# Optimization experiments

Measured on AMD Instinct MI355X. Metric: run time of the kernel, lower is better.

The kernel has to match this reference:

```python
import jax, jax.numpy as jnp
import numpy as np
import math

N, S, D, V = 8, 2048, 64, 64

def setup_inputs() -> dict:
    key = jax.random.key(0)
    k1, k2, k3, k4 = jax.random.split(key, 4)
    return {
        "queries_nqd": jax.random.normal(k1, (N, S, D), dtype=jnp.float32),
        "keys_nsd": jax.random.normal(k2, (N, S, D), dtype=jnp.float32),
        "values_nsv": jax.random.normal(k3, (N, S, V), dtype=jnp.float32),
        "prefix_len_n": jax.random.randint(k4, (N,), 0, S, dtype=jnp.int64) if jax.config.jax_enable_x64 else jax.random.randint(k4, (N,), 0, S, dtype=jnp.int32),
    }

def reference(queries_nqd, keys_nsd, values_nsv, prefix_len_n):
    n, q, d = queries_nqd.shape
    s = keys_nsd.shape[1]
    # block mask: key position < prefix_len (broadcast over query dim)  [n, q, s]
    s_idx = jnp.arange(s)
    block_mask = s_idx[None, None, :] < prefix_len_n[:, None, None]
    # diagonal mask: q == s index  [q, s]
    diag_mask = s_idx[:, None] == s_idx[None, :]
    attention_mask_nqs = block_mask | diag_mask[None, :, :]
    scores_nqs = jnp.einsum("nqd,nsd->nqs", queries_nqd, keys_nsd) / math.sqrt(d)
    scores_nqs = jnp.where(attention_mask_nqs, scores_nqs, jnp.float32(-1e9))
    probs_nqs = jax.nn.softmax(scores_nqs, axis=-1)
    # dropout p=0.0 (eval/identity)
    return jnp.einsum("nqs,nsv->nqv", probs_nqs, values_nsv)
```

## Files before the change

kernel.cpp:

```cpp
#include <hip/hip_runtime.h>
#include <cstdint>
#include <cstddef>

typedef __attribute__((ext_vector_type(8))) __bf16 bf16x8;
typedef __attribute__((ext_vector_type(2))) __bf16 bf16x2;
typedef __attribute__((ext_vector_type(4))) float f32x4;
typedef __attribute__((ext_vector_type(4))) unsigned int u32x4;

#define LOG2E 1.44269504088896340736f

constexpr int N_ = 8;
constexpr int S_ = 2048;
constexpr int D_ = 64;
constexpr int V_ = 64;
constexpr int TQ = 32;
constexpr int CK = 64;
constexpr int NW = 4;

#define GLD(d, a, OFF) \
    asm volatile("global_load_dwordx4 %0, %1, off offset:" OFF : "=&v"(d) : "v"(a))
#define WAITV(N) do { asm volatile("s_waitcnt vmcnt(" #N ")" ::: "memory"); \
                      __builtin_amdgcn_sched_barrier(0); } while (0)

__device__ __forceinline__ ushort f2bf(float x) {
    uint u = __builtin_bit_cast(uint, x);
    return (ushort)((u + 0x7FFFu + ((u >> 16) & 1u)) >> 16);
}
__device__ __forceinline__ bf16x8 bc8(const u32x4& q) {
    return __builtin_bit_cast(bf16x8, q);
}
__device__ __forceinline__ bf16x8 cvt8(const float* p, float sc) {
    f32x4 a = *reinterpret_cast<const f32x4*>(p);
    f32x4 b = *reinterpret_cast<const f32x4*>(p + 4);
    bf16x8 r;
#pragma unroll
    for (int j = 0; j < 4; j++) { r[j] = (__bf16)(a[j] * sc); r[j + 4] = (__bf16)(b[j] * sc); }
    return r;
}
__device__ __forceinline__ uint pk2(float lo, float hi) {
    bf16x2 t; t[0] = (__bf16)lo; t[1] = (__bf16)hi;
    return __builtin_bit_cast(uint, t);
}

__device__ __forceinline__ int load_prefix(const int* plen, int n) {
    bool is64 = ((plen[1] | plen[3] | plen[5] | plen[7]) == 0);
    return is64 ? plen[2 * n] : plen[n];
}

__global__ void prep_kernel(const float* __restrict__ Q, const float* __restrict__ K,
                            const float* __restrict__ V, ushort* __restrict__ Qb,
                            ushort* __restrict__ Kb, ushort* __restrict__ VTb) {
    const float QS = 0.125f * LOG2E;
    const int i4 = (blockIdx.x * 256 + threadIdx.x) * 4;
    f32x4 q = *reinterpret_cast<const f32x4*>(Q + i4);
    f32x4 k = *reinterpret_cast<const f32x4*>(K + i4);
    f32x4 v = *reinterpret_cast<const f32x4*>(V + i4);
    ushort4 qo, ko;
    qo.x = f2bf(q[0] * QS); qo.y = f2bf(q[1] * QS); qo.z = f2bf(q[2] * QS); qo.w = f2bf(q[3] * QS);
    ko.x = f2bf(k[0]); ko.y = f2bf(k[1]); ko.z = f2bf(k[2]); ko.w = f2bf(k[3]);
    *reinterpret_cast<ushort4*>(Qb + i4) = qo;
    *reinterpret_cast<ushort4*>(Kb + i4) = ko;
    const int vd = i4 & (V_ - 1);
    const int s  = (i4 >> 6) & (S_ - 1);
    const int n  = i4 >> 17;
    const size_t base = ((size_t)n * 64 + (s >> 5)) * 2048 + (s & 31);
#pragma unroll
    for (int j = 0; j < 4; j++)
        VTb[base + (size_t)(vd + j) * 32] = f2bf(v[j]);
}

template <bool WS>
__global__ __launch_bounds__(256, 2) void attn_kernel(
    const void* __restrict__ Qp, const void* __restrict__ Kp,
    const void* __restrict__ Vp, const ushort* __restrict__ VTb,
    const int* __restrict__ plen, float* __restrict__ outm)
{
    __shared__ float obuf[NW][TQ][V_ + 1];
    __shared__ float lbuf[NW][TQ];

    const int n    = blockIdx.y;
    const int q0   = blockIdx.x * TQ;
    const int tid  = threadIdx.x;
    const int w    = tid >> 6;
    const int lane = tid & 63;
    const int quad = lane >> 4;
    const int l16  = lane & 15;
    const int prefix = load_prefix(plen, n);
    const int qrow0 = q0 + l16;
    const int qrow1 = q0 + 16 + l16;

    const int krow = ((l16 >> 2) << 3) + (l16 & 3);

    bf16x8 qf00, qf01, qf10, qf11;
    if (WS) {
        const ushort* qptr = (const ushort*)Qp + ((size_t)(n * S_ + qrow0)) * D_ + quad * 8;
        uint4 u0 = *reinterpret_cast<const uint4*>(qptr);
        uint4 u1 = *reinterpret_cast<const uint4*>(qptr + 32);
        uint4 u2 = *reinterpret_cast<const uint4*>(qptr + 16 * D_);
        uint4 u3 = *reinterpret_cast<const uint4*>(qptr + 16 * D_ + 32);
        qf00 = __builtin_bit_cast(bf16x8, u0); qf01 = __builtin_bit_cast(bf16x8, u1);
        qf10 = __builtin_bit_cast(bf16x8, u2); qf11 = __builtin_bit_cast(bf16x8, u3);
    } else {
        const float* qptr = (const float*)Qp + ((size_t)(n * S_ + qrow0)) * D_ + quad * 8;
        qf00 = cvt8(qptr, 0.125f * LOG2E);            qf01 = cvt8(qptr + 32, 0.125f * LOG2E);
        qf10 = cvt8(qptr + 16 * D_, 0.125f * LOG2E);  qf11 = cvt8(qptr + 16 * D_ + 32, 0.125f * LOG2E);
    }
    asm volatile("" : "+v"(qf00), "+v"(qf01), "+v"(qf10), "+v"(qf11));

    f32x4 oa[4], ob[4];
#pragma unroll
    for (int vb = 0; vb < 4; vb++) { oa[vb] = (f32x4){0.f,0.f,0.f,0.f}; ob[vb] = (f32x4){0.f,0.f,0.f,0.f}; }
    float l0 = 0.f, l1 = 0.f;

    const float* Kf = (const float*)Kp + (size_t)n * S_ * D_;
    const float* Vf = (const float*)Vp + (size_t)n * S_ * V_;

    const uint64_t kbase0 = (uint64_t)(uintptr_t)((const ushort*)Kp)
        + (size_t)n * S_ * D_ * 2 + (size_t)krow * 128 + quad * 16;
    const uint64_t vbase0 = (uint64_t)(uintptr_t)VTb
        + (size_t)n * 64 * 2048 * 2 + (size_t)l16 * 64 + quad * 16;

    auto issueKV = [&](u32x4* f, int c) {
        const uint64_t ka = kbase0 + (uint64_t)c * (CK * 128);
        const uint64_t kb = ka + 4096;
        const uint64_t va = vbase0 + (uint64_t)c * (2 * 4096);
        const uint64_t vb = va + 4096;
        GLD(f[0],  ka, "0");   GLD(f[1],  ka, "64");
        GLD(f[2],  ka, "512"); GLD(f[3],  ka, "576");
        GLD(f[4],  kb, "0");   GLD(f[5],  kb, "64");
        GLD(f[6],  kb, "512"); GLD(f[7],  kb, "576");
        GLD(f[8],  va, "0");   GLD(f[9],  va, "1024");
        GLD(f[10], va, "2048");GLD(f[11], va, "3072");
        GLD(f[12], vb, "0");   GLD(f[13], vb, "1024");
        GLD(f[14], vb, "2048");GLD(f[15], vb, "3072");
    };

    auto computeChunk = [&](const u32x4* f, int kb, bool masked, bool wait16) {
        const f32x4 zero = (f32x4){0.f, 0.f, 0.f, 0.f};
        uint4 pw0, pw1, pw2, pw3;
        {
            f32x4 s0 = __builtin_amdgcn_mfma_f32_16x16x32_bf16(bc8(f[0]), qf00, zero, 0, 0, 0);
            s0 = __builtin_amdgcn_mfma_f32_16x16x32_bf16(bc8(f[1]), qf01, s0, 0, 0, 0);
            f32x4 s1 = __builtin_amdgcn_mfma_f32_16x16x32_bf16(bc8(f[2]), qf00, zero, 0, 0, 0);
            s1 = __builtin_amdgcn_mfma_f32_16x16x32_bf16(bc8(f[3]), qf01, s1, 0, 0, 0);
            f32x4 s2 = __builtin_amdgcn_mfma_f32_16x16x32_bf16(bc8(f[4]), qf00, zero, 0, 0, 0);
            s2 = __builtin_amdgcn_mfma_f32_16x16x32_bf16(bc8(f[5]), qf01, s2, 0, 0, 0);
            f32x4 s3 = __builtin_amdgcn_mfma_f32_16x16x32_bf16(bc8(f[6]), qf00, zero, 0, 0, 0);
            s3 = __builtin_amdgcn_mfma_f32_16x16x32_bf16(bc8(f[7]), qf01, s3, 0, 0, 0);
            if (masked) {
#pragma unroll
                for (int r = 0; r < 4; r++) {
                    const int k0 = kb + 8 * quad + r;
                    s0[r] = (k0      < prefix || k0      == qrow0) ? s0[r] : -1e30f;
                    s1[r] = (k0 + 4  < prefix || k0 + 4  == qrow0) ? s1[r] : -1e30f;
                    s2[r] = (k0 + 32 < prefix || k0 + 32 == qrow0) ? s2[r] : -1e30f;
                    s3[r] = (k0 + 36 < prefix || k0 + 36 == qrow0) ? s3[r] : -1e30f;
                }
            }
            float p0[4], p1[4], p2[4], p3[4];
#pragma unroll
            for (int r = 0; r < 4; r++) {
                p0[r] = __builtin_amdgcn_exp2f(s0[r]);
                p1[r] = __builtin_amdgcn_exp2f(s1[r]);
                p2[r] = __builtin_amdgcn_exp2f(s2[r]);
                p3[r] = __builtin_amdgcn_exp2f(s3[r]);
            }
            l0 += ((p0[0]+p0[1])+(p0[2]+p0[3])) + ((p1[0]+p1[1])+(p1[2]+p1[3]))
                + ((p2[0]+p2[1])+(p2[2]+p2[3])) + ((p3[0]+p3[1])+(p3[2]+p3[3]));
            pw0.x = pk2(p0[0], p0[1]); pw0.y = pk2(p0[2], p0[3]);
            pw0.z = pk2(p1[0], p1[1]); pw0.w = pk2(p1[2], p1[3]);
            pw1.x = pk2(p2[0], p2[1]); pw1.y = pk2(p2[2], p2[3]);
            pw1.z = pk2(p3[0], p3[1]); pw1.w = pk2(p3[2], p3[3]);
        }
        {
            f32x4 s0 = __builtin_amdgcn_mfma_f32_16x16x32_bf16(bc8(f[0]), qf10, zero, 0, 0, 0);
            s0 = __builtin_amdgcn_mfma_f32_16x16x32_bf16(bc8(f[1]), qf11, s0, 0, 0, 0);
            f32x4 s1 = __builtin_amdgcn_mfma_f32_16x16x32_bf16(bc8(f[2]), qf10, zero, 0, 0, 0);
            s1 = __builtin_amdgcn_mfma_f32_16x16x32_bf16(bc8(f[3]), qf11, s1, 0, 0, 0);
            f32x4 s2 = __builtin_amdgcn_mfma_f32_16x16x32_bf16(bc8(f[4]), qf10, zero, 0, 0, 0);
            s2 = __builtin_amdgcn_mfma_f32_16x16x32_bf16(bc8(f[5]), qf11, s2, 0, 0, 0);
            f32x4 s3 = __builtin_amdgcn_mfma_f32_16x16x32_bf16(bc8(f[6]), qf10, zero, 0, 0, 0);
            s3 = __builtin_amdgcn_mfma_f32_16x16x32_bf16(bc8(f[7]), qf11, s3, 0, 0, 0);
            if (masked) {
#pragma unroll
                for (int r = 0; r < 4; r++) {
                    const int k0 = kb + 8 * quad + r;
                    s0[r] = (k0      < prefix || k0      == qrow1) ? s0[r] : -1e30f;
                    s1[r] = (k0 + 4  < prefix || k0 + 4  == qrow1) ? s1[r] : -1e30f;
                    s2[r] = (k0 + 32 < prefix || k0 + 32 == qrow1) ? s2[r] : -1e30f;
                    s3[r] = (k0 + 36 < prefix || k0 + 36 == qrow1) ? s3[r] : -1e30f;
                }
            }
            float p0[4], p1[4], p2[4], p3[4];
#pragma unroll
            for (int r = 0; r < 4; r++) {
                p0[r] = __builtin_amdgcn_exp2f(s0[r]);
                p1[r] = __builtin_amdgcn_exp2f(s1[r]);
                p2[r] = __builtin_amdgcn_exp2f(s2[r]);
                p3[r] = __builtin_amdgcn_exp2f(s3[r]);
            }
            l1 += ((p0[0]+p0[1])+(p0[2]+p0[3])) + ((p1[0]+p1[1])+(p1[2]+p1[3]))
                + ((p2[0]+p2[1])+(p2[2]+p2[3])) + ((p3[0]+p3[1])+(p3[2]+p3[3]));
            pw2.x = pk2(p0[0], p0[1]); pw2.y = pk2(p0[2], p0[3]);
            pw2.z = pk2(p1[0], p1[1]); pw2.w = pk2(p1[2], p1[3]);
            pw3.x = pk2(p2[0], p2[1]); pw3.y = pk2(p2[2], p2[3]);
            pw3.z = pk2(p3[0], p3[1]); pw3.w = pk2(p3[2], p3[3]);
        }
        if (wait16) WAITV(16);
        const bf16x8 pA0 = __builtin_bit_cast(bf16x8, pw0);
        const bf16x8 pA1 = __builtin_bit_cast(bf16x8, pw1);
        const bf16x8 pB0 = __builtin_bit_cast(bf16x8, pw2);
        const bf16x8 pB1 = __builtin_bit_cast(bf16x8, pw3);
#pragma unroll
        for (int vb = 0; vb < 4; vb++) {
            oa[vb] = __builtin_amdgcn_mfma_f32_16x16x32_bf16(bc8(f[8 + vb]),  pA0, oa[vb], 0, 0, 0);
            oa[vb] = __builtin_amdgcn_mfma_f32_16x16x32_bf16(bc8(f[12 + vb]), pA1, oa[vb], 0, 0, 0);
            ob[vb] = __builtin_amdgcn_mfma_f32_16x16x32_bf16(bc8(f[8 + vb]),  pB0, ob[vb], 0, 0, 0);
            ob[vb] = __builtin_amdgcn_mfma_f32_16x16x32_bf16(bc8(f[12 + vb]), pB1, ob[vb], 0, 0, 0);
        }
    };

    const int nFull = prefix >> 6;
    const int nPC   = (prefix + CK - 1) >> 6;
    const int dc    = q0 >> 6;

    if (WS) {
        u32x4 bufA[16], bufB[16];
        int c = w;
        if (c < nFull) {
            issueKV(bufA, c);
            int c1 = c + NW;
            if (c1 >= nFull) {
                WAITV(0); computeChunk(bufA, c * CK, false, false);
            } else {
                issueKV(bufB, c1);
                for (;;) {
                    int c2 = c1 + NW;
                    if (c2 >= nFull) {
                        WAITV(16); computeChunk(bufA, c * CK, false, false);
                        WAITV(0);  computeChunk(bufB, c1 * CK, false, false);
                        break;
                    }
                    WAITV(24);
                    computeChunk(bufA, c * CK, false, true);
                    issueKV(bufA, c2);
                    c = c1; c1 = c2; c2 = c1 + NW;
                    if (c2 >= nFull) {
                        WAITV(16); computeChunk(bufB, c * CK, false, false);
                        WAITV(0);  computeChunk(bufA, c1 * CK, false, false);
                        break;
                    }
                    WAITV(24);
                    computeChunk(bufB, c * CK, false, true);
                    issueKV(bufB, c2);
                    c = c1; c1 = c2;
                }
            }
        }
        if (nPC > nFull && (nFull & (NW - 1)) == w) {
            issueKV(bufA, nFull); WAITV(0); computeChunk(bufA, nFull * CK, true, false);
        }
        if (dc >= nPC && (dc & (NW - 1)) == w) {
            issueKV(bufA, dc); WAITV(0); computeChunk(bufA, dc * CK, true, false);
        }
    } else {
        for (int c = w; c < nFull + 2; c++) {
            int cc; bool masked;
            if (c < nFull) { if ((c & (NW - 1)) != (w & (NW - 1)) || c >= nFull) {} }
            break;
        }
        auto computeNW = [&](int kb, bool masked) {
            u32x4 f[16];
            const float* kp = Kf + (size_t)(kb + krow) * D_ + quad * 8;
            f[0] = __builtin_bit_cast(u32x4, cvt8(kp, 1.f));
            f[1] = __builtin_bit_cast(u32x4, cvt8(kp + 32, 1.f));
            f[2] = __builtin_bit_cast(u32x4, cvt8(kp + 4 * D_, 1.f));
            f[3] = __builtin_bit_cast(u32x4, cvt8(kp + 4 * D_ + 32, 1.f));
            f[4] = __builtin_bit_cast(u32x4, cvt8(kp + 32 * D_, 1.f));
            f[5] = __builtin_bit_cast(u32x4, cvt8(kp + 32 * D_ + 32, 1.f));
            f[6] = __builtin_bit_cast(u32x4, cvt8(kp + 36 * D_, 1.f));
            f[7] = __builtin_bit_cast(u32x4, cvt8(kp + 36 * D_ + 32, 1.f));
#pragma unroll
            for (int vb = 0; vb < 4; vb++) {
                bf16x8 vf0, vf1;
#pragma unroll
                for (int j = 0; j < 8; j++) {
                    vf0[j] = (__bf16)Vf[(size_t)(kb + quad * 8 + j) * V_ + vb * 16 + l16];
                    vf1[j] = (__bf16)Vf[(size_t)(kb + 32 + quad * 8 + j) * V_ + vb * 16 + l16];
                }
                f[8 + vb]  = __builtin_bit_cast(u32x4, vf0);
                f[12 + vb] = __builtin_bit_cast(u32x4, vf1);
            }
            computeChunk(f, kb, masked, false);
        };
        for (int c = w; c < nFull; c += NW) computeNW(c * CK, false);
        if (nPC > nFull && (nFull & (NW - 1)) == w) computeNW(nFull * CK, true);
        if (dc >= nPC && (dc & (NW - 1)) == w) computeNW(dc * CK, true);
    }

#pragma unroll
    for (int vb = 0; vb < 4; vb++)
#pragma unroll
        for (int r = 0; r < 4; r++) {
            obuf[w][l16][vb * 16 + quad * 4 + r]      = oa[vb][r];
            obuf[w][16 + l16][vb * 16 + quad * 4 + r] = ob[vb][r];
        }
    l0 += __shfl_xor(l0, 16, 64);
    l0 += __shfl_xor(l0, 32, 64);
    l1 += __shfl_xor(l1, 16, 64);
    l1 += __shfl_xor(l1, 32, 64);
    if (quad == 0) { lbuf[w][l16] = l0; lbuf[w][16 + l16] = l1; }
    __syncthreads();

    const int row = tid >> 3;
    const int vd0 = (tid & 7) * 8;
    float lg = (lbuf[0][row] + lbuf[1][row]) + (lbuf[2][row] + lbuf[3][row]);
    float acc[8] = {0.f,0.f,0.f,0.f,0.f,0.f,0.f,0.f};
#pragma unroll
    for (int ww = 0; ww < NW; ww++) {
#pragma unroll
        for (int i = 0; i < 8; i++) acc[i] += obuf[ww][row][vd0 + i];
    }
    const float inv = 1.f / lg;
    f32x4 o4a = (f32x4){acc[0] * inv, acc[1] * inv, acc[2] * inv, acc[3] * inv};
    f32x4 o4b = (f32x4){acc[4] * inv, acc[5] * inv, acc[6] * inv, acc[7] * inv};
    float* op = outm + ((size_t)(n * S_ + q0 + row)) * V_ + vd0;
    *reinterpret_cast<f32x4*>(op)     = o4a;
    *reinterpret_cast<f32x4*>(op + 4) = o4b;
}

extern "C" void kernel_launch(void* const* d_in, const int* in_sizes, int n_in,
                              void* d_out, int out_size, void* d_ws, size_t ws_size,
                              hipStream_t stream) {
    const float* Qf = (const float*)d_in[0];
    const float* Kf = (const float*)d_in[1];
    const float* Vf = (const float*)d_in[2];
    const int* plen = (const int*)d_in[3];
    float* outm = (float*)d_out;

    constexpr size_t ELEMS = (size_t)N_ * S_ * D_;
    const size_t need = 3 * ELEMS * sizeof(ushort);
    dim3 agrid(S_ / TQ, N_);

    if (ws_size >= need) {
        ushort* Qb  = (ushort*)d_ws;
        ushort* Kb  = Qb + ELEMS;
        ushort* VTb = Kb + ELEMS;
        prep_kernel<<<ELEMS / (256 * 4), 256, 0, stream>>>(Qf, Kf, Vf, Qb, Kb, VTb);
        attn_kernel<true><<<agrid, 256, 0, stream>>>(Qb, Kb, nullptr, VTb, plen, outm);
    } else {
        attn_kernel<false><<<agrid, 256, 0, stream>>>(Qf, Kf, Vf, nullptr, plen, outm);
    }
}
```

Measured before the change: 91.46 us.

## Balance load by sorting batches by prefix and pairing tasks per block

The prep kernel now sorts the batch indices by prefix length and writes a task schedule. The attention kernel launches half as many blocks with 8 waves each, and each block handles two tasks: one from the front of the sorted list and one from the back, so long and short prefix workloads are paired. Global loads now use a scalar base with a 32-bit vector offset, which cuts address VGPR use. The cost is an extra barrier between the two tasks, a larger shared reduction buffer, and the loss of the 2D grid.

```diff
diff --git a/kernel.cpp b/kernel.cpp
--- a/kernel.cpp
+++ b/kernel.cpp
@@ -15,10 +15,12 @@
 constexpr int V_ = 64;
 constexpr int TQ = 32;
 constexpr int CK = 64;
-constexpr int NW = 4;
-
-#define GLD(d, a, OFF) \
-    asm volatile("global_load_dwordx4 %0, %1, off offset:" OFF : "=&v"(d) : "v"(a))
+constexpr int NW = 8;
+constexpr int NTASK = (S_ / TQ) * N_;
+
+#define GLDS(d, off, base, OFF) \
+    asm volatile("global_load_dwordx4 %0, %1, %2 offset:" OFF \
+                 : "=&v"(d) : "v"(off), "s"(base))
 #define WAITV(N) do { asm volatile("s_waitcnt vmcnt(" #N ")" ::: "memory"); \
                       __builtin_amdgcn_sched_barrier(0); } while (0)
 
@@ -49,7 +51,8 @@
 
 __global__ void prep_kernel(const float* __restrict__ Q, const float* __restrict__ K,
                             const float* __restrict__ V, ushort* __restrict__ Qb,
-                            ushort* __restrict__ Kb, ushort* __restrict__ VTb) {
+                            ushort* __restrict__ Kb, ushort* __restrict__ VTb,
+                            const int* __restrict__ plen, int* __restrict__ sched) {
     const float QS = 0.125f * LOG2E;
     const int i4 = (blockIdx.x * 256 + threadIdx.x) * 4;
     f32x4 q = *reinterpret_cast<const f32x4*>(Q + i4);
@@ -67,266 +70,288 @@
 #pragma unroll
     for (int j = 0; j < 4; j++)
         VTb[base + (size_t)(vd + j) * 32] = f2bf(v[j]);
+
+    if (blockIdx.x == 0) {
+        __shared__ int ordl[8];
+        if (threadIdx.x == 0) {
+            int pv[8];
+#pragma unroll
+            for (int i = 0; i < 8; i++) { pv[i] = load_prefix(plen, i); ordl[i] = i; }
+            for (int i = 1; i < 8; i++)
+                for (int j = i; j > 0 && pv[ordl[j]] > pv[ordl[j - 1]]; j--) {
+                    int t = ordl[j]; ordl[j] = ordl[j - 1]; ordl[j - 1] = t;
+                }
+        }
+        __syncthreads();
+        for (int t = threadIdx.x; t < NTASK; t += 256)
+            sched[t] = (ordl[t >> 6] << 16) | (t & 63);
+    }
 }
 
 template <bool WS>
-__global__ __launch_bounds__(256, 2) void attn_kernel(
+__global__ __launch_bounds__(512, 2) void attn_kernel(
     const void* __restrict__ Qp, const void* __restrict__ Kp,
     const void* __restrict__ Vp, const ushort* __restrict__ VTb,
-    const int* __restrict__ plen, float* __restrict__ outm)
+    const int* __restrict__ plen, const int* __restrict__ sched,
+    float* __restrict__ outm)
 {
     __shared__ float obuf[NW][TQ][V_ + 1];
     __shared__ float lbuf[NW][TQ];
 
-    const int n    = blockIdx.y;
-    const int q0   = blockIdx.x * TQ;
     const int tid  = threadIdx.x;
     const int w    = tid >> 6;
     const int lane = tid & 63;
     const int quad = lane >> 4;
     const int l16  = lane & 15;
-    const int prefix = load_prefix(plen, n);
-    const int qrow0 = q0 + l16;
-    const int qrow1 = q0 + 16 + l16;
-
     const int krow = ((l16 >> 2) << 3) + (l16 & 3);
-
-    bf16x8 qf00, qf01, qf10, qf11;
-    if (WS) {
-        const ushort* qptr = (const ushort*)Qp + ((size_t)(n * S_ + qrow0)) * D_ + quad * 8;
-        uint4 u0 = *reinterpret_cast<const uint4*>(qptr);
-        uint4 u1 = *reinterpret_cast<const uint4*>(qptr + 32);
-        uint4 u2 = *reinterpret_cast<const uint4*>(qptr + 16 * D_);
-        uint4 u3 = *reinterpret_cast<const uint4*>(qptr + 16 * D_ + 32);
-        qf00 = __builtin_bit_cast(bf16x8, u0); qf01 = __builtin_bit_cast(bf16x8, u1);
-        qf10 = __builtin_bit_cast(bf16x8, u2); qf11 = __builtin_bit_cast(bf16x8, u3);
-    } else {
-        const float* qptr = (const float*)Qp + ((size_t)(n * S_ + qrow0)) * D_ + quad * 8;
-        qf00 = cvt8(qptr, 0.125f * LOG2E);            qf01 = cvt8(qptr + 32, 0.125f * LOG2E);
-        qf10 = cvt8(qptr + 16 * D_, 0.125f * LOG2E);  qf11 = cvt8(qptr + 16 * D_ + 32, 0.125f * LOG2E);
+    const uint vk0 = (uint)(krow * 128 + quad * 16);
+    const uint vv0 = (uint)(l16 * 64 + quad * 16);
+
+    const int nIt = WS ? 2 : 1;
+    for (int it = 0; it < nIt; it++) {
+        int n, q0;
+        if (WS) {
+            const int entry = sched[it == 0 ? (int)blockIdx.x
+                                            : (NTASK - 1 - (int)blockIdx.x)];
+            n  = entry >> 16;
+            q0 = (entry & 0xffff) * TQ;
+        } else {
+            n  = blockIdx.y;
+            q0 = blockIdx.x * TQ;
+        }
+        __syncthreads();
+
+        const int prefix = load_prefix(plen, n);
+        const int qrow0 = q0 + l16;
+        const int qrow1 = q0 + 16 + l16;
+
+        bf16x8 qf00, qf01, qf10, qf11;
+        if (WS) {
+            const ushort* qptr = (const ushort*)Qp + ((size_t)(n * S_ + qrow0)) * D_ + quad * 8;
+            uint4 u0 = *reinterpret_cast<const uint4*>(qptr);
+            uint4 u1 = *reinterpret_cast<const uint4*>(qptr + 32);
+            uint4 u2 = *reinterpret_cast<const uint4*>(qptr + 16 * D_);
+            uint4 u3 = *reinterpret_cast<const uint4*>(qptr + 16 * D_ + 32);
+            qf00 = __builtin_bit_cast(bf16x8, u0); qf01 = __builtin_bit_cast(bf16x8, u1);
+            qf10 = __builtin_bit_cast(bf16x8, u2); qf11 = __builtin_bit_cast(bf16x8, u3);
+        } else {
+            const float* qptr = (const float*)Qp + ((size_t)(n * S_ + qrow0)) * D_ + quad * 8;
+            qf00 = cvt8(qptr, 0.125f * LOG2E);            qf01 = cvt8(qptr + 32, 0.125f * LOG2E);
+            qf10 = cvt8(qptr + 16 * D_, 0.125f * LOG2E);  qf11 = cvt8(qptr + 16 * D_ + 32, 0.125f * LOG2E);
+        }
+        asm volatile("" : "+v"(qf00), "+v"(qf01), "+v"(qf10), "+v"(qf11));
+
+        f32x4 oa[4], ob[4];
+#pragma unroll
+        for (int vb = 0; vb < 4; vb++) { oa[vb] = (f32x4){0.f,0.f,0.f,0.f}; ob[vb] = (f32x4){0.f,0.f,0.f,0.f}; }
+        float l0 = 0.f, l1 = 0.f;
+
+        const float* Kf = (const float*)Kp + (size_t)n * S_ * D_;
+        const float* Vf = (const float*)Vp + (size_t)n * S_ * V_;
+        const ushort* Kbb = (const ushort*)Kp + (size_t)n * S_ * D_;
+        const ushort* VTn = VTb + (size_t)n * 64 * 2048;
+
+        auto issueKV = [&](u32x4* f, int c) {
+            const uint ko  = vk0 + (uint)c * 8192u;
+            const uint ko2 = ko + 4096u;
+            const uint vo  = vv0 + (uint)c * 8192u;
+            const uint vo2 = vo + 4096u;
+            GLDS(f[0],  ko,  Kbb, "0");    GLDS(f[1],  ko,  Kbb, "64");
+            GLDS(f[2],  ko,  Kbb, "512");  GLDS(f[3],  ko,  Kbb, "576");
+            GLDS(f[4],  ko2, Kbb, "0");    GLDS(f[5],  ko2, Kbb, "64");
+            GLDS(f[6],  ko2, Kbb, "512");  GLDS(f[7],  ko2, Kbb, "576");
+            GLDS(f[8],  vo,  VTn, "0");    GLDS(f[9],  vo,  VTn, "1024");
+            GLDS(f[10], vo,  VTn, "2048"); GLDS(f[11], vo,  VTn, "3072");
+            GLDS(f[12], vo2, VTn, "0");    GLDS(f[13], vo2, VTn, "1024");
+            GLDS(f[14], vo2, VTn, "2048"); GLDS(f[15], vo2, VTn, "3072");
+        };
+
+        auto computeChunk = [&](const u32x4* f, int kb, bool masked, bool wait16) {
+            const f32x4 zero = (f32x4){0.f, 0.f, 0.f, 0.f};
+            uint4 pw0, pw1, pw2, pw3;
+            {
+                f32x4 s0 = __builtin_amdgcn_mfma_f32_16x16x32_bf16(bc8(f[0]), qf00, zero, 0, 0, 0);
+                s0 = __builtin_amdgcn_mfma_f32_16x16x32_bf16(bc8(f[1]), qf01, s0, 0, 0, 0);
+                f32x4 s1 = __builtin_amdgcn_mfma_f32_16x16x32_bf16(bc8(f[2]), qf00, zero, 0, 0, 0);
+                s1 = __builtin_amdgcn_mfma_f32_16x16x32_bf16(bc8(f[3]), qf01, s1, 0, 0, 0);
+                f32x4 s2 = __builtin_amdgcn_mfma_f32_16x16x32_bf16(bc8(f[4]), qf00, zero, 0, 0, 0);
+                s2 = __builtin_amdgcn_mfma_f32_16x16x32_bf16(bc8(f[5]), qf01, s2, 0, 0, 0);
+                f32x4 s3 = __builtin_amdgcn_mfma_f32_16x16x32_bf16(bc8(f[6]), qf00, zero, 0, 0, 0);
+                s3 = __builtin_amdgcn_mfma_f32_16x16x32_bf16(bc8(f[7]), qf01, s3, 0, 0, 0);
+                if (masked) {
+#pragma unroll
+                    for (int r = 0; r < 4; r++) {
+                        const int k0 = kb + 8 * quad + r;
+                        s0[r] = (k0      < prefix || k0      == qrow0) ? s0[r] : -1e30f;
+                        s1[r] = (k0 + 4  < prefix || k0 + 4  == qrow0) ? s1[r] : -1e30f;
+                        s2[r] = (k0 + 32 < prefix || k0 + 32 == qrow0) ? s2[r] : -1e30f;
+                        s3[r] = (k0 + 36 < prefix || k0 + 36 == qrow0) ? s3[r] : -1e30f;
+                    }
+                }
+                float p0[4], p1[4], p2[4], p3[4];
+#pragma unroll
+                for (int r = 0; r < 4; r++) {
+                    p0[r] = __builtin_amdgcn_exp2f(s0[r]);
+                    p1[r] = __builtin_amdgcn_exp2f(s1[r]);
+                    p2[r] = __builtin_amdgcn_exp2f(s2[r]);
+                    p3[r] = __builtin_amdgcn_exp2f(s3[r]);
+                }
+                l0 += ((p0[0]+p0[1])+(p0[2]+p0[3])) + ((p1[0]+p1[1])+(p1[2]+p1[3]))
+                    + ((p2[0]+p2[1])+(p2[2]+p2[3])) + ((p3[0]+p3[1])+(p3[2]+p3[3]));
+                pw0.x = pk2(p0[0], p0[1]); pw0.y = pk2(p0[2], p0[3]);
+                pw0.z = pk2(p1[0], p1[1]); pw0.w = pk2(p1[2], p1[3]);
+                pw1.x = pk2(p2[0], p2[1]); pw1.y = pk2(p2[2], p2[3]);
+                pw1.z = pk2(p3[0], p3[1]); pw1.w = pk2(p3[2], p3[3]);
+            }
+            {
+                f32x4 s0 = __builtin_amdgcn_mfma_f32_16x16x32_bf16(bc8(f[0]), qf10, zero, 0, 0, 0);
+                s0 = __builtin_amdgcn_mfma_f32_16x16x32_bf16(bc8(f[1]), qf11, s0, 0, 0, 0);
+                f32x4 s1 = __builtin_amdgcn_mfma_f32_16x16x32_bf16(bc8(f[2]), qf10, zero, 0, 0, 0);
+                s1 = __builtin_amdgcn_mfma_f32_16x16x32_bf16(bc8(f[3]), qf11, s1, 0, 0, 0);
+                f32x4 s2 = __builtin_amdgcn_mfma_f32_16x16x32_bf16(bc8(f[4]), qf10, zero, 0, 0, 0);
+                s2 = __builtin_amdgcn_mfma_f32_16x16x32_bf16(bc8(f[5]), qf11, s2, 0, 0, 0);
+                f32x4 s3 = __builtin_amdgcn_mfma_f32_16x16x32_bf16(bc8(f[6]), qf10, zero, 0, 0, 0);
+                s3 = __builtin_amdgcn_mfma_f32_16x16x32_bf16(bc8(f[7]), qf11, s3, 0, 0, 0);
+                if (masked) {
+#pragma unroll
+                    for (int r = 0; r < 4; r++) {
+                        const int k0 = kb + 8 * quad + r;
+                        s0[r] = (k0      < prefix || k0      == qrow1) ? s0[r] : -1e30f;
+                        s1[r] = (k0 + 4  < prefix || k0 + 4  == qrow1) ? s1[r] : -1e30f;
+                        s2[r] = (k0 + 32 < prefix || k0 + 32 == qrow1) ? s2[r] : -1e30f;
+                        s3[r] = (k0 + 36 < prefix || k0 + 36 == qrow1) ? s3[r] : -1e30f;
+                    }
+                }
+                float p0[4], p1[4], p2[4], p3[4];
+#pragma unroll
+                for (int r = 0; r < 4; r++) {
+                    p0[r] = __builtin_amdgcn_exp2f(s0[r]);
+                    p1[r] = __builtin_amdgcn_exp2f(s1[r]);
+                    p2[r] = __builtin_amdgcn_exp2f(s2[r]);
+                    p3[r] = __builtin_amdgcn_exp2f(s3[r]);
+                }
+                l1 += ((p0[0]+p0[1])+(p0[2]+p0[3])) + ((p1[0]+p1[1])+(p1[2]+p1[3]))
+                    + ((p2[0]+p2[1])+(p2[2]+p2[3])) + ((p3[0]+p3[1])+(p3[2]+p3[3]));
+                pw2.x = pk2(p0[0], p0[1]); pw2.y = pk2(p0[2], p0[3]);
+                pw2.z = pk2(p1[0], p1[1]); pw2.w = pk2(p1[2], p1[3]);
+                pw3.x = pk2(p2[0], p2[1]); pw3.y = pk2(p2[2], p2[3]);
+                pw3.z = pk2(p3[0], p3[1]); pw3.w = pk2(p3[2], p3[3]);
+            }
+            if (wait16) WAITV(16);
+            const bf16x8 pA0 = __builtin_bit_cast(bf16x8, pw0);
+            const bf16x8 pA1 = __builtin_bit_cast(bf16x8, pw1);
+            const bf16x8 pB0 = __builtin_bit_cast(bf16x8, pw2);
+            const bf16x8 pB1 = __builtin_bit_cast(bf16x8, pw3);
+#pragma unroll
+            for (int vb = 0; vb < 4; vb++) {
+                oa[vb] = __builtin_amdgcn_mfma_f32_16x16x32_bf16(bc8(f[8 + vb]),  pA0, oa[vb], 0, 0, 0);
+                oa[vb] = __builtin_amdgcn_mfma_f32_16x16x32_bf16(bc8(f[12 + vb]), pA1, oa[vb], 0, 0, 0);
+                ob[vb] = __builtin_amdgcn_mfma_f32_16x16x32_bf16(bc8(f[8 + vb]),  pB0, ob[vb], 0, 0, 0);
+                ob[vb] = __builtin_amdgcn_mfma_f32_16x16x32_bf16(bc8(f[12 + vb]), pB1, ob[vb], 0, 0, 0);
+            }
+        };
+
+        const int nFull = prefix >> 6;
+        const int nPC   = (prefix + CK - 1) >> 6;
+        const int dc    = q0 >> 6;
+
+        if (WS) {
+            u32x4 bufA[16], bufB[16];
+            int c = w;
+            if (c < nFull) {
+                issueKV(bufA, c);
+                int c1 = c + NW;
+                if (c1 >= nFull) {
+                    WAITV(0); computeChunk(bufA, c * CK, false, false);
+                } else {
+                    issueKV(bufB, c1);
+                    for (;;) {
+                        int c2 = c1 + NW;
+                        if (c2 >= nFull) {
+                            WAITV(16); computeChunk(bufA, c * CK, false, false);
+                            WAITV(0);  computeChunk(bufB, c1 * CK, false, false);
+                            break;
+                        }
+                        WAITV(24);
+                        computeChunk(bufA, c * CK, false, true);
+                        issueKV(bufA, c2);
+                        c = c1; c1 = c2; c2 = c1 + NW;
+                        if (c2 >= nFull) {
+                            WAITV(16); computeChunk(bufB, c * CK, false, false);
+                            WAITV(0);  computeChunk(bufA, c1 * CK, false, false);
+                            break;
+                        }
+                        WAITV(24);
+                        computeChunk(bufB, c * CK, false, true);
+                        issueKV(bufB, c2);
+                        c = c1; c1 = c2;
+                    }
+                }
+            }
+            if (nPC > nFull && (nFull & (NW - 1)) == w) {
+                issueKV(bufA, nFull); WAITV(0); computeChunk(bufA, nFull * CK, true, false);
+            }
+            if (dc >= nPC && (dc & (NW - 1)) == w) {
+                issueKV(bufA, dc); WAITV(0); computeChunk(bufA, dc * CK, true, false);
+            }
+        } else {
+            auto computeNW = [&](int kb, bool masked) {
+                u32x4 f[16];
+                const float* kp = Kf + (size_t)(kb + krow) * D_ + quad * 8;
+                f[0] = __builtin_bit_cast(u32x4, cvt8(kp, 1.f));
+                f[1] = __builtin_bit_cast(u32x4, cvt8(kp + 32, 1.f));
+                f[2] = __builtin_bit_cast(u32x4, cvt8(kp + 4 * D_, 1.f));
+                f[3] = __builtin_bit_cast(u32x4, cvt8(kp + 4 * D_ + 32, 1.f));
+                f[4] = __builtin_bit_cast(u32x4, cvt8(kp + 32 * D_, 1.f));
+                f[5] = __builtin_bit_cast(u32x4, cvt8(kp + 32 * D_ + 32, 1.f));
+                f[6] = __builtin_bit_cast(u32x4, cvt8(kp + 36 * D_, 1.f));
+                f[7] = __builtin_bit_cast(u32x4, cvt8(kp + 36 * D_ + 32, 1.f));
+#pragma unroll
+                for (int vb = 0; vb < 4; vb++) {
+                    bf16x8 vf0, vf1;
+#pragma unroll
+                    for (int j = 0; j < 8; j++) {
+                        vf0[j] = (__bf16)Vf[(size_t)(kb + quad * 8 + j) * V_ + vb * 16 + l16];
+                        vf1[j] = (__bf16)Vf[(size_t)(kb + 32 + quad * 8 + j) * V_ + vb * 16 + l16];
+                    }
+                    f[8 + vb]  = __builtin_bit_cast(u32x4, vf0);
+                    f[12 + vb] = __builtin_bit_cast(u32x4, vf1);
+                }
+                computeChunk(f, kb, masked, false);
+            };
+            for (int c = w; c < nFull; c += NW) computeNW(c * CK, false);
+            if (nPC > nFull && (nFull & (NW - 1)) == w) computeNW(nFull * CK, true);
+            if (dc >= nPC && (dc & (NW - 1)) == w) computeNW(dc * CK, true);
+        }
+
+#pragma unroll
+        for (int vb = 0; vb < 4; vb++)
+#pragma unroll
+            for (int r = 0; r < 4; r++) {
+                obuf[w][l16][vb * 16 + quad * 4 + r]      = oa[vb][r];
+                obuf[w][16 + l16][vb * 16 + quad * 4 + r] = ob[vb][r];
+            }
+        l0 += __shfl_xor(l0, 16, 64);
+        l0 += __shfl_xor(l0, 32, 64);
+        l1 += __shfl_xor(l1, 16, 64);
+        l1 += __shfl_xor(l1, 32, 64);
+        if (quad == 0) { lbuf[w][l16] = l0; lbuf[w][16 + l16] = l1; }
+        __syncthreads();
+
+        const int row = tid >> 4;
+        const int vd0 = (tid & 15) * 4;
+        float lg = 0.f;
+        float acc[4] = {0.f, 0.f, 0.f, 0.f};
+#pragma unroll
+        for (int ww = 0; ww < NW; ww++) {
+            lg += lbuf[ww][row];
+#pragma unroll
+            for (int i = 0; i < 4; i++) acc[i] += obuf[ww][row][vd0 + i];
+        }
+        const float inv = 1.f / lg;
+        f32x4 o4 = (f32x4){acc[0] * inv, acc[1] * inv, acc[2] * inv, acc[3] * inv};
+        *reinterpret_cast<f32x4*>(outm + ((size_t)(n * S_ + q0 + row)) * V_ + vd0) = o4;
     }
-    asm volatile("" : "+v"(qf00), "+v"(qf01), "+v"(qf10), "+v"(qf11));
-
-    f32x4 oa[4], ob[4];
-#pragma unroll
-    for (int vb = 0; vb < 4; vb++) { oa[vb] = (f32x4){0.f,0.f,0.f,0.f}; ob[vb] = (f32x4){0.f,0.f,0.f,0.f}; }
-    float l0 = 0.f, l1 = 0.f;
-
-    const float* Kf = (const float*)Kp + (size_t)n * S_ * D_;
-    const float* Vf = (const float*)Vp + (size_t)n * S_ * V_;
-
-    const uint64_t kbase0 = (uint64_t)(uintptr_t)((const ushort*)Kp)
-        + (size_t)n * S_ * D_ * 2 + (size_t)krow * 128 + quad * 16;
-    const uint64_t vbase0 = (uint64_t)(uintptr_t)VTb
-        + (size_t)n * 64 * 2048 * 2 + (size_t)l16 * 64 + quad * 16;
-
-    auto issueKV = [&](u32x4* f, int c) {
-        const uint64_t ka = kbase0 + (uint64_t)c * (CK * 128);
-        const uint64_t kb = ka + 4096;
-        const uint64_t va = vbase0 + (uint64_t)c * (2 * 4096);
-        const uint64_t vb = va + 4096;
-        GLD(f[0],  ka, "0");   GLD(f[1],  ka, "64");
-        GLD(f[2],  ka, "512"); GLD(f[3],  ka, "576");
-        GLD(f[4],  kb, "0");   GLD(f[5],  kb, "64");
-        GLD(f[6],  kb, "512"); GLD(f[7],  kb, "576");
-        GLD(f[8],  va, "0");   GLD(f[9],  va, "1024");
-        GLD(f[10], va, "2048");GLD(f[11], va, "3072");
-        GLD(f[12], vb, "0");   GLD(f[13], vb, "1024");
-        GLD(f[14], vb, "2048");GLD(f[15], vb, "3072");
-    };
-
-    auto computeChunk = [&](const u32x4* f, int kb, bool masked, bool wait16) {
-        const f32x4 zero = (f32x4){0.f, 0.f, 0.f, 0.f};
-        uint4 pw0, pw1, pw2, pw3;
-        {
-            f32x4 s0 = __builtin_amdgcn_mfma_f32_16x16x32_bf16(bc8(f[0]), qf00, zero, 0, 0, 0);
-            s0 = __builtin_amdgcn_mfma_f32_16x16x32_bf16(bc8(f[1]), qf01, s0, 0, 0, 0);
-            f32x4 s1 = __builtin_amdgcn_mfma_f32_16x16x32_bf16(bc8(f[2]), qf00, zero, 0, 0, 0);
-            s1 = __builtin_amdgcn_mfma_f32_16x16x32_bf16(bc8(f[3]), qf01, s1, 0, 0, 0);
-            f32x4 s2 = __builtin_amdgcn_mfma_f32_16x16x32_bf16(bc8(f[4]), qf00, zero, 0, 0, 0);
-            s2 = __builtin_amdgcn_mfma_f32_16x16x32_bf16(bc8(f[5]), qf01, s2, 0, 0, 0);
-            f32x4 s3 = __builtin_amdgcn_mfma_f32_16x16x32_bf16(bc8(f[6]), qf00, zero, 0, 0, 0);
-            s3 = __builtin_amdgcn_mfma_f32_16x16x32_bf16(bc8(f[7]), qf01, s3, 0, 0, 0);
-            if (masked) {
-#pragma unroll
-                for (int r = 0; r < 4; r++) {
-                    const int k0 = kb + 8 * quad + r;
-                    s0[r] = (k0      < prefix || k0      == qrow0) ? s0[r] : -1e30f;
-                    s1[r] = (k0 + 4  < prefix || k0 + 4  == qrow0) ? s1[r] : -1e30f;
-                    s2[r] = (k0 + 32 < prefix || k0 + 32 == qrow0) ? s2[r] : -1e30f;
-                    s3[r] = (k0 + 36 < prefix || k0 + 36 == qrow0) ? s3[r] : -1e30f;
-                }
-            }
-            float p0[4], p1[4], p2[4], p3[4];
-#pragma unroll
-            for (int r = 0; r < 4; r++) {
-                p0[r] = __builtin_amdgcn_exp2f(s0[r]);
-                p1[r] = __builtin_amdgcn_exp2f(s1[r]);
-                p2[r] = __builtin_amdgcn_exp2f(s2[r]);
-                p3[r] = __builtin_amdgcn_exp2f(s3[r]);
-            }
-            l0 += ((p0[0]+p0[1])+(p0[2]+p0[3])) + ((p1[0]+p1[1])+(p1[2]+p1[3]))
-                + ((p2[0]+p2[1])+(p2[2]+p2[3])) + ((p3[0]+p3[1])+(p3[2]+p3[3]));
-            pw0.x = pk2(p0[0], p0[1]); pw0.y = pk2(p0[2], p0[3]);
-            pw0.z = pk2(p1[0], p1[1]); pw0.w = pk2(p1[2], p1[3]);
-            pw1.x = pk2(p2[0], p2[1]); pw1.y = pk2(p2[2], p2[3]);
-            pw1.z = pk2(p3[0], p3[1]); pw1.w = pk2(p3[2], p3[3]);
-        }
-        {
-            f32x4 s0 = __builtin_amdgcn_mfma_f32_16x16x32_bf16(bc8(f[0]), qf10, zero, 0, 0, 0);
-            s0 = __builtin_amdgcn_mfma_f32_16x16x32_bf16(bc8(f[1]), qf11, s0, 0, 0, 0);
-            f32x4 s1 = __builtin_amdgcn_mfma_f32_16x16x32_bf16(bc8(f[2]), qf10, zero, 0, 0, 0);
-            s1 = __builtin_amdgcn_mfma_f32_16x16x32_bf16(bc8(f[3]), qf11, s1, 0, 0, 0);
-            f32x4 s2 = __builtin_amdgcn_mfma_f32_16x16x32_bf16(bc8(f[4]), qf10, zero, 0, 0, 0);
-            s2 = __builtin_amdgcn_mfma_f32_16x16x32_bf16(bc8(f[5]), qf11, s2, 0, 0, 0);
-            f32x4 s3 = __builtin_amdgcn_mfma_f32_16x16x32_bf16(bc8(f[6]), qf10, zero, 0, 0, 0);
-            s3 = __builtin_amdgcn_mfma_f32_16x16x32_bf16(bc8(f[7]), qf11, s3, 0, 0, 0);
-            if (masked) {
-#pragma unroll
-                for (int r = 0; r < 4; r++) {
-                    const int k0 = kb + 8 * quad + r;
-                    s0[r] = (k0      < prefix || k0      == qrow1) ? s0[r] : -1e30f;
-                    s1[r] = (k0 + 4  < prefix || k0 + 4  == qrow1) ? s1[r] : -1e30f;
-                    s2[r] = (k0 + 32 < prefix || k0 + 32 == qrow1) ? s2[r] : -1e30f;
-                    s3[r] = (k0 + 36 < prefix || k0 + 36 == qrow1) ? s3[r] : -1e30f;
-                }
-            }
-            float p0[4], p1[4], p2[4], p3[4];
-#pragma unroll
-            for (int r = 0; r < 4; r++) {
-                p0[r] = __builtin_amdgcn_exp2f(s0[r]);
-                p1[r] = __builtin_amdgcn_exp2f(s1[r]);
-                p2[r] = __builtin_amdgcn_exp2f(s2[r]);
-                p3[r] = __builtin_amdgcn_exp2f(s3[r]);
-            }
-            l1 += ((p0[0]+p0[1])+(p0[2]+p0[3])) + ((p1[0]+p1[1])+(p1[2]+p1[3]))
-                + ((p2[0]+p2[1])+(p2[2]+p2[3])) + ((p3[0]+p3[1])+(p3[2]+p3[3]));
-            pw2.x = pk2(p0[0], p0[1]); pw2.y = pk2(p0[2], p0[3]);
-            pw2.z = pk2(p1[0], p1[1]); pw2.w = pk2(p1[2], p1[3]);
-            pw3.x = pk2(p2[0], p2[1]); pw3.y = pk2(p2[2], p2[3]);
-            pw3.z = pk2(p3[0], p3[1]); pw3.w = pk2(p3[2], p3[3]);
-        }
-        if (wait16) WAITV(16);
-        const bf16x8 pA0 = __builtin_bit_cast(bf16x8, pw0);
-        const bf16x8 pA1 = __builtin_bit_cast(bf16x8, pw1);
-        const bf16x8 pB0 = __builtin_bit_cast(bf16x8, pw2);
-        const bf16x8 pB1 = __builtin_bit_cast(bf16x8, pw3);
-#pragma unroll
-        for (int vb = 0; vb < 4; vb++) {
-            oa[vb] = __builtin_amdgcn_mfma_f32_16x16x32_bf16(bc8(f[8 + vb]),  pA0, oa[vb], 0, 0, 0);
-            oa[vb] = __builtin_amdgcn_mfma_f32_16x16x32_bf16(bc8(f[12 + vb]), pA1, oa[vb], 0, 0, 0);
-            ob[vb] = __builtin_amdgcn_mfma_f32_16x16x32_bf16(bc8(f[8 + vb]),  pB0, ob[vb], 0, 0, 0);
-            ob[vb] = __builtin_amdgcn_mfma_f32_16x16x32_bf16(bc8(f[12 + vb]), pB1, ob[vb], 0, 0, 0);
-        }
-    };
-
-    const int nFull = prefix >> 6;
-    const int nPC   = (prefix + CK - 1) >> 6;
-    const int dc    = q0 >> 6;
-
-    if (WS) {
-        u32x4 bufA[16], bufB[16];
-        int c = w;
-        if (c < nFull) {
-            issueKV(bufA, c);
-            int c1 = c + NW;
-            if (c1 >= nFull) {
-                WAITV(0); computeChunk(bufA, c * CK, false, false);
-            } else {
-                issueKV(bufB, c1);
-                for (;;) {
-                    int c2 = c1 + NW;
-                    if (c2 >= nFull) {
-                        WAITV(16); computeChunk(bufA, c * CK, false, false);
-                        WAITV(0);  computeChunk(bufB, c1 * CK, false, false);
-                        break;
-                    }
-                    WAITV(24);
-                    computeChunk(bufA, c * CK, false, true);
-                    issueKV(bufA, c2);
-                    c = c1; c1 = c2; c2 = c1 + NW;
-                    if (c2 >= nFull) {
-                        WAITV(16); computeChunk(bufB, c * CK, false, false);
-                        WAITV(0);  computeChunk(bufA, c1 * CK, false, false);
-                        break;
-                    }
-                    WAITV(24);
-                    computeChunk(bufB, c * CK, false, true);
-                    issueKV(bufB, c2);
-                    c = c1; c1 = c2;
-                }
-            }
-        }
-        if (nPC > nFull && (nFull & (NW - 1)) == w) {
-            issueKV(bufA, nFull); WAITV(0); computeChunk(bufA, nFull * CK, true, false);
-        }
-        if (dc >= nPC && (dc & (NW - 1)) == w) {
-            issueKV(bufA, dc); WAITV(0); computeChunk(bufA, dc * CK, true, false);
-        }
-    } else {
-        for (int c = w; c < nFull + 2; c++) {
-            int cc; bool masked;
-            if (c < nFull) { if ((c & (NW - 1)) != (w & (NW - 1)) || c >= nFull) {} }
-            break;
-        }
-        auto computeNW = [&](int kb, bool masked) {
-            u32x4 f[16];
-            const float* kp = Kf + (size_t)(kb + krow) * D_ + quad * 8;
-            f[0] = __builtin_bit_cast(u32x4, cvt8(kp, 1.f));
-            f[1] = __builtin_bit_cast(u32x4, cvt8(kp + 32, 1.f));
-            f[2] = __builtin_bit_cast(u32x4, cvt8(kp + 4 * D_, 1.f));
-            f[3] = __builtin_bit_cast(u32x4, cvt8(kp + 4 * D_ + 32, 1.f));
-            f[4] = __builtin_bit_cast(u32x4, cvt8(kp + 32 * D_, 1.f));
-            f[5] = __builtin_bit_cast(u32x4, cvt8(kp + 32 * D_ + 32, 1.f));
-            f[6] = __builtin_bit_cast(u32x4, cvt8(kp + 36 * D_, 1.f));
-            f[7] = __builtin_bit_cast(u32x4, cvt8(kp + 36 * D_ + 32, 1.f));
-#pragma unroll
-            for (int vb = 0; vb < 4; vb++) {
-                bf16x8 vf0, vf1;
-#pragma unroll
-                for (int j = 0; j < 8; j++) {
-                    vf0[j] = (__bf16)Vf[(size_t)(kb + quad * 8 + j) * V_ + vb * 16 + l16];
-                    vf1[j] = (__bf16)Vf[(size_t)(kb + 32 + quad * 8 + j) * V_ + vb * 16 + l16];
-                }
-                f[8 + vb]  = __builtin_bit_cast(u32x4, vf0);
-                f[12 + vb] = __builtin_bit_cast(u32x4, vf1);
-            }
-            computeChunk(f, kb, masked, false);
-        };
-        for (int c = w; c < nFull; c += NW) computeNW(c * CK, false);
-        if (nPC > nFull && (nFull & (NW - 1)) == w) computeNW(nFull * CK, true);
-        if (dc >= nPC && (dc & (NW - 1)) == w) computeNW(dc * CK, true);
-    }
-
-#pragma unroll
-    for (int vb = 0; vb < 4; vb++)
-#pragma unroll
-        for (int r = 0; r < 4; r++) {
-            obuf[w][l16][vb * 16 + quad * 4 + r]      = oa[vb][r];
-            obuf[w][16 + l16][vb * 16 + quad * 4 + r] = ob[vb][r];
-        }
-    l0 += __shfl_xor(l0, 16, 64);
-    l0 += __shfl_xor(l0, 32, 64);
-    l1 += __shfl_xor(l1, 16, 64);
-    l1 += __shfl_xor(l1, 32, 64);
-    if (quad == 0) { lbuf[w][l16] = l0; lbuf[w][16 + l16] = l1; }
-    __syncthreads();
-
-    const int row = tid >> 3;
-    const int vd0 = (tid & 7) * 8;
-    float lg = (lbuf[0][row] + lbuf[1][row]) + (lbuf[2][row] + lbuf[3][row]);
-    float acc[8] = {0.f,0.f,0.f,0.f,0.f,0.f,0.f,0.f};
-#pragma unroll
-    for (int ww = 0; ww < NW; ww++) {
-#pragma unroll
-        for (int i = 0; i < 8; i++) acc[i] += obuf[ww][row][vd0 + i];
-    }
-    const float inv = 1.f / lg;
-    f32x4 o4a = (f32x4){acc[0] * inv, acc[1] * inv, acc[2] * inv, acc[3] * inv};
-    f32x4 o4b = (f32x4){acc[4] * inv, acc[5] * inv, acc[6] * inv, acc[7] * inv};
-    float* op = outm + ((size_t)(n * S_ + q0 + row)) * V_ + vd0;
-    *reinterpret_cast<f32x4*>(op)     = o4a;
-    *reinterpret_cast<f32x4*>(op + 4) = o4b;
 }
 
 extern "C" void kernel_launch(void* const* d_in, const int* in_sizes, int n_in,
@@ -339,16 +364,16 @@
     float* outm = (float*)d_out;
 
     constexpr size_t ELEMS = (size_t)N_ * S_ * D_;
-    const size_t need = 3 * ELEMS * sizeof(ushort);
-    dim3 agrid(S_ / TQ, N_);
+    const size_t need = 3 * ELEMS * sizeof(ushort) + NTASK * sizeof(int);
 
     if (ws_size >= need) {
         ushort* Qb  = (ushort*)d_ws;
         ushort* Kb  = Qb + ELEMS;
         ushort* VTb = Kb + ELEMS;
-        prep_kernel<<<ELEMS / (256 * 4), 256, 0, stream>>>(Qf, Kf, Vf, Qb, Kb, VTb);
-        attn_kernel<true><<<agrid, 256, 0, stream>>>(Qb, Kb, nullptr, VTb, plen, outm);
+        int*   sched = (int*)(VTb + ELEMS);
+        prep_kernel<<<ELEMS / (256 * 4), 256, 0, stream>>>(Qf, Kf, Vf, Qb, Kb, VTb, plen, sched);
+        attn_kernel<true><<<NTASK / 2, 512, 0, stream>>>(Qb, Kb, nullptr, VTb, plen, sched, outm);
     } else {
-        attn_kernel<false><<<agrid, 256, 0, stream>>>(Qf, Kf, Vf, nullptr, plen, outm);
+        attn_kernel<false><<<dim3(S_ / TQ, N_), 512, 0, stream>>>(Qf, Kf, Vf, nullptr, plen, nullptr, outm);
     }
 }
```

Result: no change. 92.26 us (+0.9%).
